# Performance work log

Hardware: AMD Instinct MI355X
Metric: run time of the kernel (lower is better)

Reference implementation:

```python
import jax, jax.numpy as jnp
import numpy as np

B, T, D_IN, H = 1024, 512, 32, 64


def setup_inputs() -> dict:
    key = jax.random.key(0)
    ks = jax.random.split(key, 16)
    s_in = 1.0 / np.sqrt(H)  # torch LSTM init scale 1/sqrt(hidden)
    inp = {
        "x": jax.random.normal(ks[0], (B, T, D_IN), dtype=jnp.float32),
        # layer 0
        "Wih0": jax.random.uniform(ks[1], (4 * H, D_IN), minval=-s_in, maxval=s_in),
        "Whh0": jax.random.uniform(ks[2], (4 * H, H), minval=-s_in, maxval=s_in),
        "bih0": jax.random.uniform(ks[3], (4 * H,), minval=-s_in, maxval=s_in),
        "bhh0": jax.random.uniform(ks[4], (4 * H,), minval=-s_in, maxval=s_in),
        # layer 1
        "Wih1": jax.random.uniform(ks[5], (4 * H, H), minval=-s_in, maxval=s_in),
        "Whh1": jax.random.uniform(ks[6], (4 * H, H), minval=-s_in, maxval=s_in),
        "bih1": jax.random.uniform(ks[7], (4 * H,), minval=-s_in, maxval=s_in),
        "bhh1": jax.random.uniform(ks[8], (4 * H,), minval=-s_in, maxval=s_in),
        # head: Linear(H, H//2) -> ReLU -> Linear(H//2, 1)
        "W1": jax.random.uniform(ks[9], (H // 2, H), minval=-s_in, maxval=s_in),
        "b1": jax.random.uniform(ks[10], (H // 2,), minval=-s_in, maxval=s_in),
        "W2": jax.random.uniform(ks[11], (1, H // 2), minval=-1.0 / np.sqrt(H // 2), maxval=1.0 / np.sqrt(H // 2)),
        "b2": jax.random.uniform(ks[12], (1,), minval=-1.0 / np.sqrt(H // 2), maxval=1.0 / np.sqrt(H // 2)),
    }
    return inp


def _lstm_layer(x, Wih, Whh, bih, bhh):
    # x: [B, T, D]; returns all hidden states [B, T, H]
    b = x.shape[0]
    xT = jnp.swapaxes(x, 0, 1)  # [T, B, D]
    h0 = jnp.zeros((b, H), dtype=x.dtype)
    c0 = jnp.zeros((b, H), dtype=x.dtype)
    bias = bih + bhh

    def step(carry, xt):
        h, c = carry
        z = xt @ Wih.T + h @ Whh.T + bias  # [B, 4H]
        i, f, g, o = jnp.split(z, 4, axis=-1)  # torch gate order: i, f, g, o
        i = jax.nn.sigmoid(i)
        f = jax.nn.sigmoid(f)
        g = jnp.tanh(g)
        o = jax.nn.sigmoid(o)
        c = f * c + i * g
        h = o * jnp.tanh(c)
        return (h, c), h

    _, hs = jax.lax.scan(step, (h0, c0), xT)
    return jnp.swapaxes(hs, 0, 1)  # [B, T, H]


def reference(x, Wih0, Whh0, bih0, bhh0, Wih1, Whh1, bih1, bhh1, W1, b1, W2, b2):
    h1 = _lstm_layer(x, Wih0, Whh0, bih0, bhh0)   # [B, T, H]
    h2 = _lstm_layer(h1, Wih1, Whh1, bih1, bhh1)  # [B, T, H] (dropout = identity, eval)
    last = h2[:, -1]                              # [B, H]
    hidden = jax.nn.relu(last @ W1.T + b1)        # [B, H//2]
    out = hidden @ W2.T + b2                      # [B, 1]
    return out[:, 0]                              # [B]
```

## Files before the change

kernel.cpp:

```cpp
#include <hip/hip_runtime.h>

#define T       512
#define DIN     32
#define HCELLS  64
#define NB      16
#define TB      512
#define GRID    64

typedef _Float16 half8  __attribute__((ext_vector_type(8)));
typedef _Float16 half4v __attribute__((ext_vector_type(4)));
typedef float    float4v __attribute__((ext_vector_type(4)));

#define STRH    72
#define H0H_OFF 0
#define H1H_OFF (2*16*STRH)
#define SB_HALFS (H1H_OFF + 2*16*STRH)

#define LOG2E   1.44269504f
#define SLOG2E  2.88539008f

#define BARRIER() asm volatile("s_waitcnt lgkmcnt(0)\n\ts_barrier" ::: "memory")

__device__ __forceinline__ int hidx(int p, int n, int k) { return (p * 16 + n) * STRH + k; }

__device__ __forceinline__ void cvt8(const float* v, half8& hi) {
    #pragma unroll
    for (int e = 0; e < 8; ++e) hi[e] = (_Float16)v[e];
}

__device__ __forceinline__ void cell_update(const float4v acc[4], float* cs,
                                            half4v& hh, float* hout)
{
    #pragma unroll
    for (int r = 0; r < 4; ++r) {
        float ei = __builtin_amdgcn_exp2f(acc[0][r]);
        float ef = __builtin_amdgcn_exp2f(acc[1][r]);
        float G2 = __builtin_amdgcn_exp2f(acc[2][r]);
        float I  = 1.0f + ei, F = 1.0f + ef;
        float Gp = 1.0f + G2;
        float Gms = fmaf(SLOG2E, G2, -SLOG2E);
        float P   = I * Gp;
        float num = fmaf(F, Gms, cs[r] * P);
        float csn = num * __builtin_amdgcn_rcpf(F * P);
        csn = fminf(fmaxf(csn, -50.0f), 50.0f);
        cs[r] = csn;
        float eo = __builtin_amdgcn_exp2f(acc[3][r]);
        float C2 = __builtin_amdgcn_exp2f(csn);
        float O  = 1.0f + eo;
        float Cp = 1.0f + C2, Cm = C2 - 1.0f;
        float h  = Cm * __builtin_amdgcn_rcpf(O * Cp);
        if (hout) hout[r] = h;
        hh[r] = (_Float16)h;
    }
}

__global__ void __launch_bounds__(TB, 2)
lstm2_mfma_kernel(const float* __restrict__ x,
                  const float* __restrict__ Wih0, const float* __restrict__ Whh0,
                  const float* __restrict__ bih0, const float* __restrict__ bhh0,
                  const float* __restrict__ Wih1, const float* __restrict__ Whh1,
                  const float* __restrict__ bih1, const float* __restrict__ bhh1,
                  const float* __restrict__ W1,   const float* __restrict__ b1,
                  const float* __restrict__ W2,   const float* __restrict__ b2,
                  float* __restrict__ out)
{
    const int tid  = threadIdx.x;
    const int wid  = tid >> 6;
    const int grp  = wid >> 2;
    const int wl   = wid & 3;
    const int lane = tid & 63;
    const int n16  = lane & 15;
    const int q    = lane >> 4;
    const int j0   = wl * 16 + q * 4;
    const int b0   = blockIdx.x * NB;

    __shared__ __align__(16) _Float16 SB[SB_HALFS];
    __shared__ __align__(16) float HS[16 * 68 + 16 * 33];

    const float gsc[4] = {-LOG2E, -LOG2E, SLOG2E, -LOG2E};

    half8 ah[4][4];
    float4v biasv[4];

    #pragma unroll
    for (int l = 0; l < 4; ++l) {
        const int row = (l * 4 + wl) * 16 + n16;
        const float g = gsc[l];
        float v[8];
        if (grp == 0) {
            {
                const float4* p = (const float4*)(Wih0 + row * DIN + q * 8);
                float4 u0 = p[0], u1 = p[1];
                v[0]=g*u0.x; v[1]=g*u0.y; v[2]=g*u0.z; v[3]=g*u0.w;
                v[4]=g*u1.x; v[5]=g*u1.y; v[6]=g*u1.z; v[7]=g*u1.w;
                cvt8(v, ah[l][0]);
            }
            #pragma unroll
            for (int kt = 1; kt < 3; ++kt) {
                const float4* p = (const float4*)(Whh0 + row * HCELLS + (kt - 1) * 32 + q * 8);
                float4 u0 = p[0], u1 = p[1];
                v[0]=g*u0.x; v[1]=g*u0.y; v[2]=g*u0.z; v[3]=g*u0.w;
                v[4]=g*u1.x; v[5]=g*u1.y; v[6]=g*u1.z; v[7]=g*u1.w;
                cvt8(v, ah[l][kt]);
            }
            const int r0 = l * 64 + j0;
            float4v bi = *(const float4v*)(bih0 + r0);
            float4v bh = *(const float4v*)(bhh0 + r0);
            biasv[l] = (bi + bh) * g;
        } else {
            #pragma unroll
            for (int kt = 0; kt < 4; ++kt) {
                const float* base = (kt < 2) ? (Wih1 + row * HCELLS + kt * 32)
                                             : (Whh1 + row * HCELLS + (kt - 2) * 32);
                const float4* p = (const float4*)(base + q * 8);
                float4 u0 = p[0], u1 = p[1];
                v[0]=g*u0.x; v[1]=g*u0.y; v[2]=g*u0.z; v[3]=g*u0.w;
                v[4]=g*u1.x; v[5]=g*u1.y; v[6]=g*u1.z; v[7]=g*u1.w;
                cvt8(v, ah[l][kt]);
            }
            const int r0 = l * 64 + j0;
            float4v bi = *(const float4v*)(bih1 + r0);
            float4v bh = *(const float4v*)(bhh1 + r0);
            biasv[l] = (bi + bh) * g;
        }
    }

    for (int i = tid; i < SB_HALFS / 2; i += TB) ((int*)SB)[i] = 0;

    const float* xq = nullptr;
    float4 xn0, xn1;
    if (grp == 0) {
        xq = x + ((size_t)(b0 + n16) * T) * DIN + q * 8;
        xn0 = *(const float4*)xq;
        xn1 = *(const float4*)(xq + 4);
        xq += DIN;
    }

    __syncthreads();

    float cs[4] = {0, 0, 0, 0};
    float hlast[4];

    #pragma unroll 2
    for (int t = 0; t < T; ++t) {
        const int pr = t & 1, pw = pr ^ 1;

        if (grp == 0) {
            float4 xc0 = xn0, xc1 = xn1;
            if (t + 1 < T) { xn0 = *(const float4*)xq; xn1 = *(const float4*)(xq + 4); xq += DIN; }

            half8 bhx;
            bhx[0]=(_Float16)xc0.x; bhx[1]=(_Float16)xc0.y; bhx[2]=(_Float16)xc0.z; bhx[3]=(_Float16)xc0.w;
            bhx[4]=(_Float16)xc1.x; bhx[5]=(_Float16)xc1.y; bhx[6]=(_Float16)xc1.z; bhx[7]=(_Float16)xc1.w;

            float4v acc[4];
            #pragma unroll
            for (int l = 0; l < 4; ++l)
                acc[l] = __builtin_amdgcn_mfma_f32_16x16x32_f16(ah[l][0], bhx, biasv[l], 0, 0, 0);
            #pragma unroll
            for (int kt = 1; kt < 3; ++kt) {
                half8 bh = *(const half8*)&SB[H0H_OFF + hidx(pr, n16, (kt - 1) * 32 + q * 8)];
                #pragma unroll
                for (int l = 0; l < 4; ++l)
                    acc[l] = __builtin_amdgcn_mfma_f32_16x16x32_f16(ah[l][kt], bh, acc[l], 0, 0, 0);
            }
            half4v hh;
            cell_update(acc, cs, hh, nullptr);
            *(half4v*)&SB[H0H_OFF + hidx(pw, n16, j0)] = hh;
        } else if (t > 0) {
            float4v acc[4];
            #pragma unroll
            for (int l = 0; l < 4; ++l) acc[l] = biasv[l];
            #pragma unroll
            for (int kt = 0; kt < 4; ++kt) {
                half8 bh = (kt < 2)
                    ? *(const half8*)&SB[H0H_OFF + hidx(pr, n16, kt * 32 + q * 8)]
                    : *(const half8*)&SB[H1H_OFF + hidx(pw, n16, (kt - 2) * 32 + q * 8)];
                #pragma unroll
                for (int l = 0; l < 4; ++l)
                    acc[l] = __builtin_amdgcn_mfma_f32_16x16x32_f16(ah[l][kt], bh, acc[l], 0, 0, 0);
            }
            half4v hh;
            cell_update(acc, cs, hh, nullptr);
            *(half4v*)&SB[H1H_OFF + hidx(pr, n16, j0)] = hh;
        }
        BARRIER();
    }

    float* h1f = HS;
    float* hid = HS + 16 * 68;
    if (grp == 1) {
        float4v acc[4];
        #pragma unroll
        for (int l = 0; l < 4; ++l) acc[l] = biasv[l];
        #pragma unroll
        for (int kt = 0; kt < 4; ++kt) {
            half8 bh = (kt < 2)
                ? *(const half8*)&SB[H0H_OFF + hidx(0, n16, kt * 32 + q * 8)]
                : *(const half8*)&SB[H1H_OFF + hidx(1, n16, (kt - 2) * 32 + q * 8)];
            #pragma unroll
            for (int l = 0; l < 4; ++l)
                acc[l] = __builtin_amdgcn_mfma_f32_16x16x32_f16(ah[l][kt], bh, acc[l], 0, 0, 0);
        }
        half4v hh;
        cell_update(acc, cs, hh, hlast);
        *(float4*)&h1f[n16 * 68 + j0] = *(const float4*)hlast;
    }
    __syncthreads();

    if (tid < 256) {
        const int n2 = tid >> 4, m = tid & 15;
        float s0 = b1[m], s1 = b1[m + 16];
        const float* w0p = W1 + m * HCELLS;
        const float* w1p = W1 + (m + 16) * HCELLS;
        #pragma unroll
        for (int j = 0; j < HCELLS; ++j) {
            float hv = h1f[n2 * 68 + j];
            s0 = fmaf(w0p[j], hv, s0);
            s1 = fmaf(w1p[j], hv, s1);
        }
        hid[n2 * 33 + m]      = fmaxf(s0, 0.0f);
        hid[n2 * 33 + m + 16] = fmaxf(s1, 0.0f);
    }
    __syncthreads();

    if (tid < NB) {
        float s = b2[0];
        #pragma unroll
        for (int m = 0; m < 32; ++m) s = fmaf(W2[m], hid[tid * 33 + m], s);
        out[b0 + tid] = s;
    }
}

extern "C" void kernel_launch(void* const* d_in, const int* in_sizes, int n_in,
                              void* d_out, int out_size, void* d_ws, size_t ws_size,
                              hipStream_t stream) {
    const float* x    = (const float*)d_in[0];
    const float* Wih0 = (const float*)d_in[1];
    const float* Whh0 = (const float*)d_in[2];
    const float* bih0 = (const float*)d_in[3];
    const float* bhh0 = (const float*)d_in[4];
    const float* Wih1 = (const float*)d_in[5];
    const float* Whh1 = (const float*)d_in[6];
    const float* bih1 = (const float*)d_in[7];
    const float* bhh1 = (const float*)d_in[8];
    const float* W1   = (const float*)d_in[9];
    const float* b1   = (const float*)d_in[10];
    const float* W2   = (const float*)d_in[11];
    const float* b2   = (const float*)d_in[12];
    float* out = (float*)d_out;

    hipLaunchKernelGGL(lstm2_mfma_kernel, dim3(GRID), dim3(TB), 0, stream,
                       x, Wih0, Whh0, bih0, bhh0, Wih1, Whh1, bih1, bhh1,
                       W1, b1, W2, b2, out);
}
```

Before: 455.0 us.

## Split LSTM layers into producer/consumer blocks pipelined through global memory flags

Replaces the single block per batch slice, which ran both layers in lockstep, with two separate 256-thread blocks per slice. Layer 0 streams its fp16 hidden states to a workspace and publishes chunk progress through release/acquire atomic flags. Layer 1 spin-waits on each chunk, then reads those states, so the two recurrences overlap across blocks and each block's per-step barrier covers fewer waves. This needs a large workspace and all 128 blocks resident at once to avoid deadlock, and it adds global-memory traffic and polling latency; a fallback path keeps the old kernel when the workspace is too small.

Result: no change. 460.8 us (+1.3%).

```diff
diff --git a/kernel.cpp b/kernel.cpp
--- a/kernel.cpp
+++ b/kernel.cpp
@@ -4,22 +4,27 @@
 #define DIN     32
 #define HCELLS  64
 #define NB      16
-#define TB      512
-#define GRID    64
+#define NSLICE  64
+#define TB      256
+#define CH      16
+#define NCH     (T / CH)
 
 typedef _Float16 half8  __attribute__((ext_vector_type(8)));
 typedef _Float16 half4v __attribute__((ext_vector_type(4)));
 typedef float    float4v __attribute__((ext_vector_type(4)));
 
 #define STRH    72
-#define H0H_OFF 0
-#define H1H_OFF (2*16*STRH)
-#define SB_HALFS (H1H_OFF + 2*16*STRH)
+#define SB_HALFS (2*16*STRH)
 
 #define LOG2E   1.44269504f
 #define SLOG2E  2.88539008f
 
 #define BARRIER() asm volatile("s_waitcnt lgkmcnt(0)\n\ts_barrier" ::: "memory")
+
+#define WS_FLAG_BYTES 4096
+#define H0T   (16 * HCELLS)
+#define H0S   ((size_t)T * H0T)
+#define WS_NEED (WS_FLAG_BYTES + (size_t)NSLICE * H0S * sizeof(_Float16))
 
 __device__ __forceinline__ int hidx(int p, int n, int k) { return (p * 16 + n) * STRH + k; }
 
@@ -54,15 +59,232 @@
     }
 }
 
-__global__ void __launch_bounds__(TB, 2)
-lstm2_mfma_kernel(const float* __restrict__ x,
+__global__ void __launch_bounds__(TB, 1)
+lstm2_pipe_kernel(const float* __restrict__ x,
                   const float* __restrict__ Wih0, const float* __restrict__ Whh0,
                   const float* __restrict__ bih0, const float* __restrict__ bhh0,
                   const float* __restrict__ Wih1, const float* __restrict__ Whh1,
                   const float* __restrict__ bih1, const float* __restrict__ bhh1,
                   const float* __restrict__ W1,   const float* __restrict__ b1,
                   const float* __restrict__ W2,   const float* __restrict__ b2,
+                  unsigned* __restrict__ prog, _Float16* __restrict__ h0g,
                   float* __restrict__ out)
+{
+    const int tid  = threadIdx.x;
+    const int wl   = tid >> 6;
+    const int lane = tid & 63;
+    const int n16  = lane & 15;
+    const int q    = lane >> 4;
+    const int j0   = wl * 16 + q * 4;
+
+    const int g     = blockIdx.x;
+    const int role  = (g >> 3) & 1;
+    const int slice = ((g >> 4) << 3) | (g & 7);
+    const int b0    = slice * NB;
+
+    __shared__ __align__(16) _Float16 SB[SB_HALFS];
+    __shared__ __align__(16) float HS[16 * 68 + 16 * 33];
+
+    const float gsc[4] = {-LOG2E, -LOG2E, SLOG2E, -LOG2E};
+
+    half8 ah[4][4];
+    float4v biasv[4];
+
+    #pragma unroll
+    for (int l = 0; l < 4; ++l) {
+        const int row = (l * 4 + wl) * 16 + n16;
+        const float g2 = gsc[l];
+        float v[8];
+        if (role == 0) {
+            {
+                const float4* p = (const float4*)(Wih0 + row * DIN + q * 8);
+                float4 u0 = p[0], u1 = p[1];
+                v[0]=g2*u0.x; v[1]=g2*u0.y; v[2]=g2*u0.z; v[3]=g2*u0.w;
+                v[4]=g2*u1.x; v[5]=g2*u1.y; v[6]=g2*u1.z; v[7]=g2*u1.w;
+                cvt8(v, ah[l][0]);
+            }
+            #pragma unroll
+            for (int kt = 1; kt < 3; ++kt) {
+                const float4* p = (const float4*)(Whh0 + row * HCELLS + (kt - 1) * 32 + q * 8);
+                float4 u0 = p[0], u1 = p[1];
+                v[0]=g2*u0.x; v[1]=g2*u0.y; v[2]=g2*u0.z; v[3]=g2*u0.w;
+                v[4]=g2*u1.x; v[5]=g2*u1.y; v[6]=g2*u1.z; v[7]=g2*u1.w;
+                cvt8(v, ah[l][kt]);
+            }
+            const int r0 = l * 64 + j0;
+            float4v bi = *(const float4v*)(bih0 + r0);
+            float4v bh = *(const float4v*)(bhh0 + r0);
+            biasv[l] = (bi + bh) * g2;
+        } else {
+            #pragma unroll
+            for (int kt = 0; kt < 4; ++kt) {
+                const float* base = (kt < 2) ? (Wih1 + row * HCELLS + kt * 32)
+                                             : (Whh1 + row * HCELLS + (kt - 2) * 32);
+                const float4* p = (const float4*)(base + q * 8);
+                float4 u0 = p[0], u1 = p[1];
+                v[0]=g2*u0.x; v[1]=g2*u0.y; v[2]=g2*u0.z; v[3]=g2*u0.w;
+                v[4]=g2*u1.x; v[5]=g2*u1.y; v[6]=g2*u1.z; v[7]=g2*u1.w;
+                cvt8(v, ah[l][kt]);
+            }
+            const int r0 = l * 64 + j0;
+            float4v bi = *(const float4v*)(bih1 + r0);
+            float4v bh = *(const float4v*)(bhh1 + r0);
+            biasv[l] = (bi + bh) * g2;
+        }
+    }
+
+    for (int i = tid; i < SB_HALFS / 2; i += TB) ((int*)SB)[i] = 0;
+    __syncthreads();
+
+    float cs[4] = {0, 0, 0, 0};
+    float hlast[4];
+
+    if (role == 0) {
+        const float* xq = x + ((size_t)(b0 + n16) * T) * DIN + q * 8;
+        float4 xn0 = ((const float4*)xq)[0];
+        float4 xn1 = ((const float4*)xq)[1];
+        xq += DIN;
+
+        _Float16* hstream = h0g + (size_t)slice * H0S + n16 * HCELLS + j0;
+
+        for (int t = 0; t < T; ++t) {
+            const int pr = t & 1, pw = pr ^ 1;
+
+            float4 xc0 = xn0, xc1 = xn1;
+            if (t + 1 < T) { xn0 = ((const float4*)xq)[0]; xn1 = ((const float4*)xq)[1]; xq += DIN; }
+
+            half8 bhx;
+            bhx[0]=(_Float16)xc0.x; bhx[1]=(_Float16)xc0.y; bhx[2]=(_Float16)xc0.z; bhx[3]=(_Float16)xc0.w;
+            bhx[4]=(_Float16)xc1.x; bhx[5]=(_Float16)xc1.y; bhx[6]=(_Float16)xc1.z; bhx[7]=(_Float16)xc1.w;
+
+            float4v acc[4];
+            #pragma unroll
+            for (int l = 0; l < 4; ++l)
+                acc[l] = __builtin_amdgcn_mfma_f32_16x16x32_f16(ah[l][0], bhx, biasv[l], 0, 0, 0);
+            #pragma unroll
+            for (int kt = 1; kt < 3; ++kt) {
+                half8 bh = *(const half8*)&SB[hidx(pr, n16, (kt - 1) * 32 + q * 8)];
+                #pragma unroll
+                for (int l = 0; l < 4; ++l)
+                    acc[l] = __builtin_amdgcn_mfma_f32_16x16x32_f16(ah[l][kt], bh, acc[l], 0, 0, 0);
+            }
+            half4v hh;
+            cell_update(acc, cs, hh, nullptr);
+            *(half4v*)&SB[hidx(pw, n16, j0)] = hh;
+            *(half4v*)(hstream + (size_t)t * H0T) = hh;
+
+            if ((t & (CH - 1)) == (CH - 1)) {
+                __syncthreads();
+                if (tid == 0)
+                    __hip_atomic_store(prog + slice, (unsigned)(t / CH + 1),
+                                       __ATOMIC_RELEASE, __HIP_MEMORY_SCOPE_AGENT);
+            } else {
+                BARRIER();
+            }
+        }
+        return;
+    }
+
+    const _Float16* gbase = h0g + (size_t)slice * H0S + n16 * HCELLS;
+    const int ka = q * 8, kb = 32 + q * 8;
+
+    half8 a_cur, b_cur;
+    for (int c = 0; c < NCH; ++c) {
+        if (tid == 0) {
+            unsigned v;
+            while ((v = __hip_atomic_load(prog + slice, __ATOMIC_ACQUIRE,
+                                          __HIP_MEMORY_SCOPE_AGENT)) < (unsigned)(c + 1))
+                __builtin_amdgcn_s_sleep(8);
+        }
+        __syncthreads();
+
+        {
+            const _Float16* p0 = gbase + (size_t)(c * CH) * H0T;
+            a_cur = *(const half8*)(p0 + ka);
+            b_cur = *(const half8*)(p0 + kb);
+        }
+
+        for (int i = 0; i < CH; ++i) {
+            const int t = c * CH + i;
+
+            half8 a_nxt, b_nxt;
+            if (i + 1 < CH) {
+                const _Float16* pn = gbase + (size_t)(t + 1) * H0T;
+                a_nxt = *(const half8*)(pn + ka);
+                b_nxt = *(const half8*)(pn + kb);
+            }
+
+            const int sr = (t + 1) & 1;
+            const int sw = t & 1;
+
+            float4v acc[4];
+            #pragma unroll
+            for (int l = 0; l < 4; ++l)
+                acc[l] = __builtin_amdgcn_mfma_f32_16x16x32_f16(ah[l][0], a_cur, biasv[l], 0, 0, 0);
+            #pragma unroll
+            for (int l = 0; l < 4; ++l)
+                acc[l] = __builtin_amdgcn_mfma_f32_16x16x32_f16(ah[l][1], b_cur, acc[l], 0, 0, 0);
+            half8 c1 = *(const half8*)&SB[hidx(sr, n16, q * 8)];
+            half8 c2 = *(const half8*)&SB[hidx(sr, n16, 32 + q * 8)];
+            #pragma unroll
+            for (int l = 0; l < 4; ++l)
+                acc[l] = __builtin_amdgcn_mfma_f32_16x16x32_f16(ah[l][2], c1, acc[l], 0, 0, 0);
+            #pragma unroll
+            for (int l = 0; l < 4; ++l)
+                acc[l] = __builtin_amdgcn_mfma_f32_16x16x32_f16(ah[l][3], c2, acc[l], 0, 0, 0);
+
+            half4v hh;
+            cell_update(acc, cs, hh, hlast);
+            *(half4v*)&SB[hidx(sw, n16, j0)] = hh;
+            BARRIER();
+
+            a_cur = a_nxt; b_cur = b_nxt;
+        }
+    }
+
+    float* h1f = HS;
+    float* hid = HS + 16 * 68;
+    *(float4*)&h1f[n16 * 68 + j0] = *(const float4*)hlast;
+    __syncthreads();
+
+    {
+        const int n2 = tid >> 4, m = tid & 15;
+        float s0 = b1[m], s1 = b1[m + 16];
+        const float* w0p = W1 + m * HCELLS;
+        const float* w1p = W1 + (m + 16) * HCELLS;
+        #pragma unroll
+        for (int j = 0; j < HCELLS; ++j) {
+            float hv = h1f[n2 * 68 + j];
+            s0 = fmaf(w0p[j], hv, s0);
+            s1 = fmaf(w1p[j], hv, s1);
+        }
+        hid[n2 * 33 + m]      = fmaxf(s0, 0.0f);
+        hid[n2 * 33 + m + 16] = fmaxf(s1, 0.0f);
+    }
+    __syncthreads();
+
+    if (tid < NB) {
+        float s = b2[0];
+        #pragma unroll
+        for (int m = 0; m < 32; ++m) s = fmaf(W2[m], hid[tid * 33 + m], s);
+        out[b0 + tid] = s;
+    }
+}
+
+#define TBF     512
+#define FB_H0   0
+#define FB_H1   (2*16*STRH)
+#define FB_HALFS (FB_H1 + 2*16*STRH)
+
+__global__ void __launch_bounds__(TBF, 2)
+lstm2_mfma_fallback(const float* __restrict__ x,
+                    const float* __restrict__ Wih0, const float* __restrict__ Whh0,
+                    const float* __restrict__ bih0, const float* __restrict__ bhh0,
+                    const float* __restrict__ Wih1, const float* __restrict__ Whh1,
+                    const float* __restrict__ bih1, const float* __restrict__ bhh1,
+                    const float* __restrict__ W1,   const float* __restrict__ b1,
+                    const float* __restrict__ W2,   const float* __restrict__ b2,
+                    float* __restrict__ out)
 {
     const int tid  = threadIdx.x;
     const int wid  = tid >> 6;
@@ -74,11 +296,10 @@
     const int j0   = wl * 16 + q * 4;
     const int b0   = blockIdx.x * NB;
 
-    __shared__ __align__(16) _Float16 SB[SB_HALFS];
+    __shared__ __align__(16) _Float16 SB[FB_HALFS];
     __shared__ __align__(16) float HS[16 * 68 + 16 * 33];
 
     const float gsc[4] = {-LOG2E, -LOG2E, SLOG2E, -LOG2E};
-
     half8 ah[4][4];
     float4v biasv[4];
 
@@ -125,7 +346,7 @@
         }
     }
 
-    for (int i = tid; i < SB_HALFS / 2; i += TB) ((int*)SB)[i] = 0;
+    for (int i = tid; i < FB_HALFS / 2; i += TBF) ((int*)SB)[i] = 0;
 
     const float* xq = nullptr;
     float4 xn0, xn1;
@@ -135,7 +356,6 @@
         xn1 = *(const float4*)(xq + 4);
         xq += DIN;
     }
-
     __syncthreads();
 
     float cs[4] = {0, 0, 0, 0};
@@ -144,29 +364,26 @@
     #pragma unroll 2
     for (int t = 0; t < T; ++t) {
         const int pr = t & 1, pw = pr ^ 1;
-
         if (grp == 0) {
             float4 xc0 = xn0, xc1 = xn1;
             if (t + 1 < T) { xn0 = *(const float4*)xq; xn1 = *(const float4*)(xq + 4); xq += DIN; }
-
             half8 bhx;
             bhx[0]=(_Float16)xc0.x; bhx[1]=(_Float16)xc0.y; bhx[2]=(_Float16)xc0.z; bhx[3]=(_Float16)xc0.w;
             bhx[4]=(_Float16)xc1.x; bhx[5]=(_Float16)xc1.y; bhx[6]=(_Float16)xc1.z; bhx[7]=(_Float16)xc1.w;
-
             float4v acc[4];
             #pragma unroll
             for (int l = 0; l < 4; ++l)
                 acc[l] = __builtin_amdgcn_mfma_f32_16x16x32_f16(ah[l][0], bhx, biasv[l], 0, 0, 0);
             #pragma unroll
             for (int kt = 1; kt < 3; ++kt) {
-                half8 bh = *(const half8*)&SB[H0H_OFF + hidx(pr, n16, (kt - 1) * 32 + q * 8)];
+                half8 bh = *(const half8*)&SB[FB_H0 + hidx(pr, n16, (kt - 1) * 32 + q * 8)];
                 #pragma unroll
                 for (int l = 0; l < 4; ++l)
                     acc[l] = __builtin_amdgcn_mfma_f32_16x16x32_f16(ah[l][kt], bh, acc[l], 0, 0, 0);
             }
             half4v hh;
             cell_update(acc, cs, hh, nullptr);
-            *(half4v*)&SB[H0H_OFF + hidx(pw, n16, j0)] = hh;
+            *(half4v*)&SB[FB_H0 + hidx(pw, n16, j0)] = hh;
         } else if (t > 0) {
             float4v acc[4];
             #pragma unroll
@@ -174,15 +391,15 @@
             #pragma unroll
             for (int kt = 0; kt < 4; ++kt) {
                 half8 bh = (kt < 2)
-                    ? *(const half8*)&SB[H0H_OFF + hidx(pr, n16, kt * 32 + q * 8)]
-                    : *(const half8*)&SB[H1H_OFF + hidx(pw, n16, (kt - 2) * 32 + q * 8)];
+                    ? *(const half8*)&SB[FB_H0 + hidx(pr, n16, kt * 32 + q * 8)]
+                    : *(const half8*)&SB[FB_H1 + hidx(pw, n16, (kt - 2) * 32 + q * 8)];
                 #pragma unroll
                 for (int l = 0; l < 4; ++l)
                     acc[l] = __builtin_amdgcn_mfma_f32_16x16x32_f16(ah[l][kt], bh, acc[l], 0, 0, 0);
             }
             half4v hh;
             cell_update(acc, cs, hh, nullptr);
-            *(half4v*)&SB[H1H_OFF + hidx(pr, n16, j0)] = hh;
+            *(half4v*)&SB[FB_H1 + hidx(pr, n16, j0)] = hh;
         }
         BARRIER();
     }
@@ -196,8 +413,8 @@
         #pragma unroll
         for (int kt = 0; kt < 4; ++kt) {
             half8 bh = (kt < 2)
-                ? *(const half8*)&SB[H0H_OFF + hidx(0, n16, kt * 32 + q * 8)]
-                : *(const half8*)&SB[H1H_OFF + hidx(1, n16, (kt - 2) * 32 + q * 8)];
+                ? *(const half8*)&SB[FB_H0 + hidx(0, n16, kt * 32 + q * 8)]
+                : *(const half8*)&SB[FB_H1 + hidx(1, n16, (kt - 2) * 32 + q * 8)];
             #pragma unroll
             for (int l = 0; l < 4; ++l)
                 acc[l] = __builtin_amdgcn_mfma_f32_16x16x32_f16(ah[l][kt], bh, acc[l], 0, 0, 0);
@@ -250,7 +467,16 @@
     const float* b2   = (const float*)d_in[12];
     float* out = (float*)d_out;
 
-    hipLaunchKernelGGL(lstm2_mfma_kernel, dim3(GRID), dim3(TB), 0, stream,
-                       x, Wih0, Whh0, bih0, bhh0, Wih1, Whh1, bih1, bhh1,
-                       W1, b1, W2, b2, out);
+    if (d_ws != nullptr && ws_size >= WS_NEED) {
+        hipMemsetAsync(d_ws, 0, WS_FLAG_BYTES, stream);
+        unsigned*  prog = (unsigned*)d_ws;
+        _Float16*  h0g  = (_Float16*)((char*)d_ws + WS_FLAG_BYTES);
+        hipLaunchKernelGGL(lstm2_pipe_kernel, dim3(2 * NSLICE), dim3(TB), 0, stream,
+                           x, Wih0, Whh0, bih0, bhh0, Wih1, Whh1, bih1, bhh1,
+                           W1, b1, W2, b2, prog, h0g, out);
+    } else {
+        hipLaunchKernelGGL(lstm2_mfma_fallback, dim3(NSLICE), dim3(TBF), 0, stream,
+                           x, Wih0, Whh0, bih0, bhh0, Wih1, Whh1, bih1, bhh1,
+                           W1, b1, W2, b2, out);
+    }
 }
```
